# Optimization experiments

Measured on AMD Instinct MI355X. Metric: run time of the kernel, lower is better.

The kernel has to match this reference:

```python
import jax, jax.numpy as jnp
import numpy as np
from jax import lax

# pywt db8 decomposition low-pass filter (dec_lo), 16 taps
DB8_DEC_LO = jnp.array([
    -0.00011747678400228192, 0.0006754494059985568, -0.0003917403729959771,
    -0.00487035299301066, 0.008746094047015655, 0.013981027917015516,
    -0.04408825393106472, -0.01736930100202211, 0.128747426620186,
    0.00047248457399797254, -0.2840155429624281, -0.015829105256023893,
    0.5853546836548691, 0.6756307362980128, 0.3128715909144659,
    0.05441584224308161], dtype=jnp.float32)

FLEN = 16


def dwt2_ll(x):
    """LL band of pywt.dwt2(x, 'db8', mode='symmetric') for x [B,C,H,W].
    pywt dwt along an axis == symmetric pad by flen-1, full correlation with
    reversed dec_lo, take every other sample starting at offset 1."""
    B, C, H, W = x.shape
    f = DB8_DEC_LO[::-1]  # np.convolve flips the filter -> correlate with reversed
    xr = x.reshape(B * C, 1, H, W)
    # along W
    p = jnp.pad(xr, ((0, 0), (0, 0), (0, 0), (FLEN - 1, FLEN - 1)), mode='symmetric')[..., 1:]
    y = lax.conv_general_dilated(p, f.reshape(1, 1, 1, FLEN), (1, 2), 'VALID',
                                 dimension_numbers=('NCHW', 'OIHW', 'NCHW'))
    # along H
    p = jnp.pad(y, ((0, 0), (0, 0), (FLEN - 1, FLEN - 1), (0, 0)), mode='symmetric')[:, :, 1:, :]
    z = lax.conv_general_dilated(p, f.reshape(1, 1, FLEN, 1), (2, 1), 'VALID',
                                 dimension_numbers=('NCHW', 'OIHW', 'NCHW'))
    return z.reshape(B, C, z.shape[2], z.shape[3])


def setup_inputs() -> dict:
    key = jax.random.key(0)
    k1, k2, k3, k4 = jax.random.split(key, 4)
    B, C, H, W = 8, 128, 256, 256
    r = 16
    x = jax.random.normal(k1, (B, C, H, W), jnp.float32)
    conv_w = jax.random.normal(k2, (1, 2, 7, 7), jnp.float32) * 0.1  # SpatialAttention conv, no bias
    fc_w1 = jax.random.normal(k3, (C // r, C), jnp.float32) * (1.0 / np.sqrt(C))
    fc_w2 = jax.random.normal(k4, (C, C // r), jnp.float32) * (1.0 / np.sqrt(C // r))
    weight = jnp.array(0.0, dtype=jnp.float32)  # learnable fusion scalar
    return {"x": x, "conv_w": conv_w, "fc_w1": fc_w1, "fc_w2": fc_w2, "weight": weight}


def reference(x, conv_w, fc_w1, fc_w2, weight):
    # --- spatial attention ---
    avg = jnp.mean(x, axis=1, keepdims=True)
    mx = jnp.max(x, axis=1, keepdims=True)
    s = jnp.concatenate([avg, mx], axis=1)  # [B,2,H,W]
    attn = jax.nn.sigmoid(lax.conv_general_dilated(
        s, conv_w, (1, 1), ((3, 3), (3, 3)),
        dimension_numbers=('NCHW', 'OIHW', 'NCHW')))  # [B,1,H,W]
    spatial_out = x * attn
    # --- wavelet (frequency) attention; LL detached in the original ---
    ll = lax.stop_gradient(dwt2_ll(x))  # [B,C,H',W']
    y = jnp.mean(ll, axis=(2, 3))  # global avg pool -> [B,C]
    h = jax.nn.relu(y @ fc_w1.T)
    w = jax.nn.sigmoid(h @ fc_w2.T)[:, :, None, None]  # [B,C,1,1]
    wavelet_out = x * w
    # --- gated fusion ---
    alpha = jax.nn.sigmoid(weight)
    out = alpha * spatial_out + (1.0 - alpha) * wavelet_out
    return out, attn, w, alpha
```

## Files before the change

kernel.cpp:

```cpp
#include <hip/hip_runtime.h>
#include <math.h>

#define BB 8
#define CC 128
#define HH 256
#define WW 256
#define HWD 65536
#define NOUT (67108864)

#define ATTN_OFF ((size_t)NOUT)
#define W_OFF (ATTN_OFF + (size_t)BB * HWD)
#define ALPHA_OFF (W_OFF + (size_t)BB * CC)

__constant__ float g_declo[16] = {
    -0.00011747678400228192f, 0.0006754494059985568f, -0.0003917403729959771f,
    -0.00487035299301066f,    0.008746094047015655f,  0.013981027917015516f,
    -0.04408825393106472f,    -0.01736930100202211f,  0.128747426620186f,
    0.00047248457399797254f,  -0.2840155429624281f,   -0.015829105256023893f,
    0.5853546836548691f,      0.6756307362980128f,    0.3128715909144659f,
    0.05441584224308161f};

__device__ __forceinline__ float sigmoidf_(float v) {
    return 1.0f / (1.0f + expf(-v));
}

__global__ void compute_a_kernel(float* __restrict__ a_arr) {
    int t = threadIdx.x;
    float acc = 0.0f;
    for (int j = 0; j < 135; ++j) {
        for (int k = 0; k < 16; ++k) {
            int idx = 2 * j + k - 14;
            int s = (idx < 0) ? (-1 - idx) : ((idx >= WW) ? (511 - idx) : idx);
            if (s == t) acc += g_declo[15 - k];
        }
    }
    a_arr[t] = acc;
}

__global__ __launch_bounds__(256) void pass1_kernel(
    const float* __restrict__ x, const float* __restrict__ a_arr,
    float* __restrict__ avg_s, float* __restrict__ max_s,
    float* __restrict__ partial) {
    const int blk = blockIdx.x;
    const int b = blk >> 8;
    const int h = blk & 255;
    const int tid = threadIdx.x;
    const int wv = tid >> 6;
    const int lane = tid & 63;

    __shared__ float dotc[CC];
    __shared__ __align__(16) float lsum[4][256];
    __shared__ __align__(16) float lmax[4][256];

    const float4 a4 = reinterpret_cast<const float4*>(a_arr)[lane];
    const float ah = a_arr[h];

    float4 sum4 = {0.f, 0.f, 0.f, 0.f};
    float4 max4 = {-INFINITY, -INFINITY, -INFINITY, -INFINITY};

    const size_t base = (size_t)b * CC * HWD + (size_t)h * WW;
    for (int ccc = 0; ccc < 32; ++ccc) {
        const int c = wv * 32 + ccc;
        const float4 v =
            reinterpret_cast<const float4*>(x + base + (size_t)c * HWD)[lane];
        float dot = a4.x * v.x + a4.y * v.y + a4.z * v.z + a4.w * v.w;
#pragma unroll
        for (int off = 32; off >= 1; off >>= 1)
            dot += __shfl_down(dot, off, 64);
        if (lane == 0) dotc[c] = dot;
        sum4.x += v.x; sum4.y += v.y; sum4.z += v.z; sum4.w += v.w;
        max4.x = fmaxf(max4.x, v.x); max4.y = fmaxf(max4.y, v.y);
        max4.z = fmaxf(max4.z, v.z); max4.w = fmaxf(max4.w, v.w);
    }
    reinterpret_cast<float4*>(&lsum[wv][0])[lane] = sum4;
    reinterpret_cast<float4*>(&lmax[wv][0])[lane] = max4;
    __syncthreads();

    const int col = tid;
    float s = lsum[0][col] + lsum[1][col] + lsum[2][col] + lsum[3][col];
    float m = fmaxf(fmaxf(lmax[0][col], lmax[1][col]),
                    fmaxf(lmax[2][col], lmax[3][col]));
    const size_t po = (size_t)b * HWD + (size_t)h * WW + col;
    avg_s[po] = s * (1.0f / 128.0f);
    max_s[po] = m;
    if (tid < CC) partial[(size_t)blk * CC + tid] = dotc[tid] * ah;
}

__global__ __launch_bounds__(128) void mlp_kernel(
    const float* __restrict__ partial, const float* __restrict__ fc_w1,
    const float* __restrict__ fc_w2, const float* __restrict__ weight,
    float* __restrict__ w_out, float* __restrict__ alpha_out) {
    const int b = blockIdx.x;
    const int c = threadIdx.x;
    float acc = 0.0f;
    for (int h = 0; h < HH; ++h)
        acc += partial[((size_t)(b * HH + h)) * CC + c];
    const float y = acc * (1.0f / (135.0f * 135.0f));

    __shared__ float ysh[CC];
    __shared__ float hsh[8];
    ysh[c] = y;
    __syncthreads();
    if (c < 8) {
        float ha = 0.0f;
        for (int k = 0; k < CC; ++k) ha += ysh[k] * fc_w1[c * CC + k];
        hsh[c] = fmaxf(ha, 0.0f);
    }
    __syncthreads();
    float wa = 0.0f;
#pragma unroll
    for (int i = 0; i < 8; ++i) wa += hsh[i] * fc_w2[c * 8 + i];
    w_out[b * CC + c] = sigmoidf_(wa);
    if (b == 0 && c == 0) alpha_out[0] = sigmoidf_(weight[0]);
}

__global__ __launch_bounds__(256) void conv_attn_kernel(
    const float* __restrict__ avg_s, const float* __restrict__ max_s,
    const float* __restrict__ cw, float* __restrict__ attn_out) {
    const int blk = blockIdx.x;
    const int b = blk >> 8;
    const int h = blk & 255;
    const int w = threadIdx.x;

    __shared__ float k0[49], k1[49];
    if (threadIdx.x < 49) {
        k0[threadIdx.x] = cw[threadIdx.x];
        k1[threadIdx.x] = cw[49 + threadIdx.x];
    }
    __syncthreads();

    const float* A = avg_s + (size_t)b * HWD;
    const float* M = max_s + (size_t)b * HWD;
    float acc = 0.0f;
    for (int kh = 0; kh < 7; ++kh) {
        const int ih = h + kh - 3;
        if (ih < 0 || ih >= HH) continue;
        for (int kw = 0; kw < 7; ++kw) {
            const int iw = w + kw - 3;
            if (iw < 0 || iw >= WW) continue;
            const float a = A[ih * WW + iw];
            const float m = M[ih * WW + iw];
            acc = fmaf(k0[kh * 7 + kw], a, acc);
            acc = fmaf(k1[kh * 7 + kw], m, acc);
        }
    }
    attn_out[(size_t)b * HWD + (size_t)h * WW + w] = sigmoidf_(acc);
}

__global__ __launch_bounds__(256) void final_mix_kernel(
    const float* __restrict__ x, const float* __restrict__ attn,
    const float* __restrict__ wvec, const float* __restrict__ weight,
    float* __restrict__ out) {
    const size_t i4 = (size_t)blockIdx.x * 256 + threadIdx.x;
    const size_t flat = i4 * 4;
    const int b = (int)(flat >> 23);
    const int rem = (int)(flat & ((1u << 23) - 1));
    const int c = rem >> 16;
    const int hw = rem & (HWD - 1);

    const float alpha = sigmoidf_(weight[0]);
    const float wc = (1.0f - alpha) * wvec[b * CC + c];

    const float4 x4 = reinterpret_cast<const float4*>(x)[i4];
    const float4 a4 =
        *reinterpret_cast<const float4*>(attn + (size_t)b * HWD + hw);
    float4 o;
    o.x = x4.x * fmaf(alpha, a4.x, wc);
    o.y = x4.y * fmaf(alpha, a4.y, wc);
    o.z = x4.z * fmaf(alpha, a4.z, wc);
    o.w = x4.w * fmaf(alpha, a4.w, wc);
    reinterpret_cast<float4*>(out)[i4] = o;
}

extern "C" void kernel_launch(void* const* d_in, const int* in_sizes, int n_in,
                              void* d_out, int out_size, void* d_ws,
                              size_t ws_size, hipStream_t stream) {
    const float* x = (const float*)d_in[0];
    const float* conv_w = (const float*)d_in[1];
    const float* fc_w1 = (const float*)d_in[2];
    const float* fc_w2 = (const float*)d_in[3];
    const float* weight = (const float*)d_in[4];

    float* out = (float*)d_out;
    float* attn_out = out + ATTN_OFF;
    float* w_out = out + W_OFF;
    float* alpha_out = out + ALPHA_OFF;

    float* wsf = (float*)d_ws;
    float* a_arr = wsf;
    float* avg_s = wsf + 256;
    float* max_s = avg_s + (size_t)BB * HWD;
    float* partial = max_s + (size_t)BB * HWD;

    compute_a_kernel<<<1, 256, 0, stream>>>(a_arr);
    pass1_kernel<<<BB * HH, 256, 0, stream>>>(x, a_arr, avg_s, max_s, partial);
    mlp_kernel<<<BB, 128, 0, stream>>>(partial, fc_w1, fc_w2, weight, w_out,
                                       alpha_out);
    conv_attn_kernel<<<BB * HH, 256, 0, stream>>>(avg_s, max_s, conv_w,
                                                  attn_out);
    final_mix_kernel<<<NOUT / 4 / 256, 256, 0, stream>>>(x, attn_out, w_out,
                                                         weight, out);
}
```

Measured before the change: 558.4 us.

## Process four rows per block in pass1 and defer wavefront dot reductions

Each pass1 block now handles four image rows instead of one, so each wave keeps 32 per-channel dot accumulators that are weighted by the row coefficient. The cross-lane shuffle reduction then runs once per channel rather than once per channel-row. This cuts shuffle work and raises the number of loads in flight per thread. The partial array shrinks to 64 entries per batch, and the mlp reduction is updated to match. The grid drops to 512 blocks and register pressure rises, which may lower occupancy. compute_a_kernel is also simplified to closed-form index checks, but it runs once and is negligible.

```diff
diff --git a/kernel.cpp b/kernel.cpp
--- a/kernel.cpp
+++ b/kernel.cpp
@@ -7,6 +7,7 @@
 #define WW 256
 #define HWD 65536
 #define NOUT (67108864)
+#define RPB 4
 
 #define ATTN_OFF ((size_t)NOUT)
 #define W_OFF (ATTN_OFF + (size_t)BB * HWD)
@@ -25,14 +26,15 @@
 }
 
 __global__ void compute_a_kernel(float* __restrict__ a_arr) {
-    int t = threadIdx.x;
+    const int t = threadIdx.x;
     float acc = 0.0f;
     for (int j = 0; j < 135; ++j) {
-        for (int k = 0; k < 16; ++k) {
-            int idx = 2 * j + k - 14;
-            int s = (idx < 0) ? (-1 - idx) : ((idx >= WW) ? (511 - idx) : idx);
-            if (s == t) acc += g_declo[15 - k];
-        }
+        int k = t + 14 - 2 * j;
+        if (k >= 0 && k < 16) acc += g_declo[15 - k];
+        k = 13 - t - 2 * j;
+        if (k >= 0 && k < 16) acc += g_declo[15 - k];
+        k = 525 - t - 2 * j;
+        if (k >= 0 && k < 16) acc += g_declo[15 - k];
     }
     a_arr[t] = acc;
 }
@@ -41,49 +43,76 @@
     const float* __restrict__ x, const float* __restrict__ a_arr,
     float* __restrict__ avg_s, float* __restrict__ max_s,
     float* __restrict__ partial) {
-    const int blk = blockIdx.x;
-    const int b = blk >> 8;
-    const int h = blk & 255;
+    const int bid = blockIdx.x;
+    const int b = bid >> 6;
+    const int h0 = (bid & 63) * RPB;
     const int tid = threadIdx.x;
     const int wv = tid >> 6;
     const int lane = tid & 63;
 
     __shared__ float dotc[CC];
-    __shared__ __align__(16) float lsum[4][256];
-    __shared__ __align__(16) float lmax[4][256];
+    __shared__ __align__(16) float sbuf[4][RPB][WW];
+    __shared__ __align__(16) float mbuf[4][RPB][WW];
 
     const float4 a4 = reinterpret_cast<const float4*>(a_arr)[lane];
-    const float ah = a_arr[h];
-
-    float4 sum4 = {0.f, 0.f, 0.f, 0.f};
-    float4 max4 = {-INFINITY, -INFINITY, -INFINITY, -INFINITY};
-
-    const size_t base = (size_t)b * CC * HWD + (size_t)h * WW;
+    float ah[RPB];
+#pragma unroll
+    for (int r = 0; r < RPB; ++r) ah[r] = a_arr[h0 + r];
+
+    float dotacc[32];
+#pragma unroll
+    for (int i = 0; i < 32; ++i) dotacc[i] = 0.0f;
+    float4 s4[RPB], m4[RPB];
+#pragma unroll
+    for (int r = 0; r < RPB; ++r) {
+        s4[r] = make_float4(0.f, 0.f, 0.f, 0.f);
+        m4[r] = make_float4(-INFINITY, -INFINITY, -INFINITY, -INFINITY);
+    }
+
+    const float* xb = x + ((size_t)(b * CC) << 16) + ((size_t)h0 << 8);
+#pragma unroll
     for (int ccc = 0; ccc < 32; ++ccc) {
-        const int c = wv * 32 + ccc;
-        const float4 v =
-            reinterpret_cast<const float4*>(x + base + (size_t)c * HWD)[lane];
-        float dot = a4.x * v.x + a4.y * v.y + a4.z * v.z + a4.w * v.w;
-#pragma unroll
-        for (int off = 32; off >= 1; off >>= 1)
-            dot += __shfl_down(dot, off, 64);
-        if (lane == 0) dotc[c] = dot;
-        sum4.x += v.x; sum4.y += v.y; sum4.z += v.z; sum4.w += v.w;
-        max4.x = fmaxf(max4.x, v.x); max4.y = fmaxf(max4.y, v.y);
-        max4.z = fmaxf(max4.z, v.z); max4.w = fmaxf(max4.w, v.w);
-    }
-    reinterpret_cast<float4*>(&lsum[wv][0])[lane] = sum4;
-    reinterpret_cast<float4*>(&lmax[wv][0])[lane] = max4;
-    __syncthreads();
-
-    const int col = tid;
-    float s = lsum[0][col] + lsum[1][col] + lsum[2][col] + lsum[3][col];
-    float m = fmaxf(fmaxf(lmax[0][col], lmax[1][col]),
-                    fmaxf(lmax[2][col], lmax[3][col]));
-    const size_t po = (size_t)b * HWD + (size_t)h * WW + col;
-    avg_s[po] = s * (1.0f / 128.0f);
-    max_s[po] = m;
-    if (tid < CC) partial[(size_t)blk * CC + tid] = dotc[tid] * ah;
+        const float* xc = xb + ((size_t)(wv * 32 + ccc) << 16);
+#pragma unroll
+        for (int r = 0; r < RPB; ++r) {
+            const float4 v =
+                reinterpret_cast<const float4*>(xc + (r << 8))[lane];
+            dotacc[ccc] = fmaf(
+                ah[r], a4.x * v.x + a4.y * v.y + a4.z * v.z + a4.w * v.w,
+                dotacc[ccc]);
+            s4[r].x += v.x; s4[r].y += v.y; s4[r].z += v.z; s4[r].w += v.w;
+            m4[r].x = fmaxf(m4[r].x, v.x); m4[r].y = fmaxf(m4[r].y, v.y);
+            m4[r].z = fmaxf(m4[r].z, v.z); m4[r].w = fmaxf(m4[r].w, v.w);
+        }
+    }
+
+#pragma unroll
+    for (int r = 0; r < RPB; ++r) {
+        reinterpret_cast<float4*>(&sbuf[wv][r][0])[lane] = s4[r];
+        reinterpret_cast<float4*>(&mbuf[wv][r][0])[lane] = m4[r];
+    }
+
+#pragma unroll
+    for (int ccc = 0; ccc < 32; ++ccc) {
+        float d = dotacc[ccc];
+#pragma unroll
+        for (int off = 1; off < 64; off <<= 1) d += __shfl_xor(d, off, 64);
+        if (lane == 0) dotc[wv * 32 + ccc] = d;
+    }
+    __syncthreads();
+
+#pragma unroll
+    for (int r = 0; r < RPB; ++r) {
+        const int col = tid;
+        const float s = sbuf[0][r][col] + sbuf[1][r][col] + sbuf[2][r][col] +
+                        sbuf[3][r][col];
+        const float m = fmaxf(fmaxf(mbuf[0][r][col], mbuf[1][r][col]),
+                              fmaxf(mbuf[2][r][col], mbuf[3][r][col]));
+        const size_t po = ((size_t)b << 16) + ((size_t)(h0 + r) << 8) + col;
+        avg_s[po] = s * (1.0f / 128.0f);
+        max_s[po] = m;
+    }
+    if (tid < CC) partial[(size_t)bid * CC + tid] = dotc[tid];
 }
 
 __global__ __launch_bounds__(128) void mlp_kernel(
@@ -93,8 +122,8 @@
     const int b = blockIdx.x;
     const int c = threadIdx.x;
     float acc = 0.0f;
-    for (int h = 0; h < HH; ++h)
-        acc += partial[((size_t)(b * HH + h)) * CC + c];
+    for (int hb = 0; hb < 64; ++hb)
+        acc += partial[((size_t)(b * 64 + hb)) * CC + c];
     const float y = acc * (1.0f / (135.0f * 135.0f));
 
     __shared__ float ysh[CC];
@@ -138,10 +167,8 @@
         for (int kw = 0; kw < 7; ++kw) {
             const int iw = w + kw - 3;
             if (iw < 0 || iw >= WW) continue;
-            const float a = A[ih * WW + iw];
-            const float m = M[ih * WW + iw];
-            acc = fmaf(k0[kh * 7 + kw], a, acc);
-            acc = fmaf(k1[kh * 7 + kw], m, acc);
+            acc = fmaf(k0[kh * 7 + kw], A[ih * WW + iw], acc);
+            acc = fmaf(k1[kh * 7 + kw], M[ih * WW + iw], acc);
         }
     }
     attn_out[(size_t)b * HWD + (size_t)h * WW + w] = sigmoidf_(acc);
@@ -193,7 +220,8 @@
     float* partial = max_s + (size_t)BB * HWD;
 
     compute_a_kernel<<<1, 256, 0, stream>>>(a_arr);
-    pass1_kernel<<<BB * HH, 256, 0, stream>>>(x, a_arr, avg_s, max_s, partial);
+    pass1_kernel<<<BB * (HH / RPB), 256, 0, stream>>>(x, a_arr, avg_s, max_s,
+                                                      partial);
     mlp_kernel<<<BB, 128, 0, stream>>>(partial, fc_w1, fc_w2, weight, w_out,
                                        alpha_out);
     conv_attn_kernel<<<BB * HH, 256, 0, stream>>>(avg_s, max_s, conv_w,
```

Measured after the change: 559.1 us. No clear change (+0.1%).
